# Kernel tuning notes

Measured on AMD Instinct MI355X. Metric: run time of the kernel, lower is better.

## Reference

```python
import jax, jax.numpy as jnp
import numpy as np

EPS = 1e-5

def _instance_norm(t):
    # torch .var(dim=2) default is unbiased (ddof=1) over flattened HW
    b, c, h, w = t.shape
    flat = t.reshape(b, c, h * w)
    mean = flat.mean(axis=2)
    var = flat.var(axis=2, ddof=1) + EPS
    return (t - mean[:, :, None, None]) / jnp.sqrt(var)[:, :, None, None]

def _conv1x1(t, w, b):
    # w: [Cout, Cin], b: [Cout]; t: [B, Cin, H, W]
    return jnp.einsum('oc,bchw->bohw', w, t) + b[None, :, None, None]


def setup_inputs() -> dict:
    key = jax.random.key(0)
    ks = jax.random.split(key, 11)
    B, C, H, W = 4, 512, 64, 64
    scale = 1.0 / np.sqrt(C)
    inp = {
        'c': jax.random.normal(ks[0], (B, C, H, W), jnp.float32),
        's': jax.random.normal(ks[1], (B, C, H, W), jnp.float32),
        'x': jax.random.normal(ks[2], (B, C, H, W), jnp.float32),
        'c_w': jax.random.normal(ks[3], (C, C), jnp.float32) * scale,
        'c_b': jax.random.normal(ks[4], (C,), jnp.float32) * 0.01,
        's_w': jax.random.normal(ks[5], (C, C), jnp.float32) * scale,
        's_b': jax.random.normal(ks[6], (C,), jnp.float32) * 0.01,
        'i_w': jax.random.normal(ks[7], (C, C), jnp.float32) * scale,
        'i_b': jax.random.normal(ks[8], (C,), jnp.float32) * 0.01,
        'o_w': jax.random.normal(ks[9], (C, C), jnp.float32) * scale,
        'o_b': jax.random.normal(ks[10], (C,), jnp.float32) * 0.01,
    }
    return inp


def reference(c, s, x, c_w, c_b, s_w, s_b, i_w, i_b, o_w, o_b):
    B, C, H, W = c.shape
    N = H * W
    cf = _conv1x1(_instance_norm(c), c_w, c_b).reshape(B, C, N)
    sf = _conv1x1(_instance_norm(s), s_w, s_b).reshape(B, C, N)
    xf = _conv1x1(s, i_w, i_b).reshape(B, C, N)
    # mask[b, n, m] = sum_c cf[b, c, n] * sf[b, c, m]; softmax over m
    mask = jax.nn.softmax(jnp.einsum('bcn,bcm->bnm', cf, sf), axis=-1)
    # of = xf @ mask^T : of[b, c, n] = sum_m xf[b, c, m] * mask[b, n, m]
    of = jnp.einsum('bcm,bnm->bcn', xf, mask).reshape(B, C, H, W)
    of = _conv1x1(of, o_w, o_b)
    return x + of
```

## Files before the change

kernel.cpp:

```cpp
#include <hip/hip_runtime.h>

typedef unsigned short u16;
typedef _Float16 f16x8 __attribute__((ext_vector_type(8)));
typedef float f32x4 __attribute__((ext_vector_type(4)));
typedef u16 u16x4 __attribute__((ext_vector_type(4)));
typedef u16 u16x8v __attribute__((ext_vector_type(8)));

__device__ __forceinline__ u16 f2h(float f) {
    _Float16 h = (_Float16)f;
    return __builtin_bit_cast(u16, h);
}
__device__ __forceinline__ float h2f(u16 u) {
    return (float)__builtin_bit_cast(_Float16, u);
}

__global__ void __launch_bounds__(256) stats_kernel(
    const float* __restrict__ c, const float* __restrict__ s,
    float* __restrict__ mC, float* __restrict__ rC,
    float* __restrict__ mS, float* __restrict__ rS)
{
    const float* src = (blockIdx.y ? s : c) + (size_t)blockIdx.x * 4096;
    int t = threadIdx.x, lane = t & 63, wv = t >> 6;
    const float4* p = (const float4*)src;
    float sum = 0.f, sq = 0.f;
#pragma unroll
    for (int i = 0; i < 4; ++i) {
        float4 v = p[t + 256 * i];
        sum += v.x + v.y + v.z + v.w;
        sq  += v.x * v.x + v.y * v.y + v.z * v.z + v.w * v.w;
    }
#pragma unroll
    for (int m = 1; m < 64; m <<= 1) {
        sum += __shfl_xor(sum, m);
        sq  += __shfl_xor(sq, m);
    }
    __shared__ float sa[4], sb[4];
    if (!lane) { sa[wv] = sum; sb[wv] = sq; }
    __syncthreads();
    if (t == 0) {
        float S = sa[0] + sa[1] + sa[2] + sa[3];
        float Q = sb[0] + sb[1] + sb[2] + sb[3];
        float mean = S * (1.0f / 4096.0f);
        float var = (Q - 4096.0f * mean * mean) * (1.0f / 4095.0f);
        float rstd = rsqrtf(var + 1e-5f);
        if (blockIdx.y) { mS[blockIdx.x] = mean; rS[blockIdx.x] = rstd; }
        else            { mC[blockIdx.x] = mean; rC[blockIdx.x] = rstd; }
    }
}

__global__ void __launch_bounds__(256) packall(
    const float* __restrict__ c, const float* __restrict__ s,
    const float* __restrict__ mC, const float* __restrict__ rC,
    const float* __restrict__ mS, const float* __restrict__ rS,
    u16* __restrict__ cnT, u16* __restrict__ snT, u16* __restrict__ sRT)
{
    __shared__ float tile[32][33];
    int z = blockIdx.z;
    bool isS = z >= 4;
    int b = isS ? z - 4 : z;
    const float* src  = isS ? s : c;
    const float* mean = isS ? mS : mC;
    const float* rstd = isS ? rS : rC;
    u16* dh = isS ? snT : cnT;
    int n0 = blockIdx.x * 32, c0 = blockIdx.y * 32;
    int tx = threadIdx.x, ty = threadIdx.y;
    const float* sbp = src + ((size_t)b * 512 + c0) * 4096 + n0;
#pragma unroll
    for (int it = 0; it < 4; ++it) {
        int cc = ty + it * 8;
        tile[cc][tx] = sbp[(size_t)cc * 4096 + tx];
    }
    __syncthreads();
    int ch = c0 + tx;
    float mn = mean[b * 512 + ch];
    float rs = rstd[b * 512 + ch];
    size_t obase = ((size_t)b * 4096 + n0) * 512 + c0;
#pragma unroll
    for (int it = 0; it < 4; ++it) {
        int r = ty + it * 8;
        float v = tile[tx][r];
        size_t o = obase + (size_t)r * 512 + tx;
        dh[o] = f2h((v - mn) * rs);
        if (isS) sRT[o] = f2h(v);
    }
}

__global__ void __launch_bounds__(256) prep_kernel(
    const float* __restrict__ c_w, const float* __restrict__ s_w,
    const float* __restrict__ i_w, const float* __restrict__ o_w,
    u16* __restrict__ cwT, u16* __restrict__ swT,
    u16* __restrict__ iwT, u16* __restrict__ ow)
{
    int z = blockIdx.z;
    int tx = threadIdx.x, ty = threadIdx.y;
    if (z == 3) {
        size_t base = ((size_t)(blockIdx.y * 16 + blockIdx.x) * 256 +
                       (ty * 32 + tx)) * 4;
        float4 v = *(const float4*)(o_w + base);
        u16x4 o;
        o[0] = f2h(v.x); o[1] = f2h(v.y); o[2] = f2h(v.z); o[3] = f2h(v.w);
        *(u16x4*)(ow + base) = o;
        return;
    }
    const float* w = (z == 0) ? c_w : (z == 1) ? s_w : i_w;
    u16* wT = (z == 0) ? cwT : (z == 1) ? swT : iwT;
    __shared__ float tile[32][33];
    int c0 = blockIdx.x * 32, k0 = blockIdx.y * 32;
#pragma unroll
    for (int it = 0; it < 4; ++it) {
        int kk = ty + it * 8;
        tile[kk][tx] = w[(size_t)(k0 + kk) * 512 + c0 + tx];
    }
    __syncthreads();
#pragma unroll
    for (int it = 0; it < 4; ++it) {
        int r = ty + it * 8;
        wT[(size_t)(c0 + r) * 512 + k0 + tx] = f2h(tile[tx][r]);
    }
}

__global__ void __launch_bounds__(256) bias_prep(
    const float* __restrict__ o_w, const float* __restrict__ i_b,
    const float* __restrict__ o_b, const float* __restrict__ s_w,
    const float* __restrict__ c_b, float* __restrict__ v,
    float* __restrict__ wu)
{
    __shared__ float buf[512];
    int t = threadIdx.x;
    bool isWu = blockIdx.x >= 2;
    const float* vec = isWu ? c_b : i_b;
    buf[t] = vec[t]; buf[t + 256] = vec[t + 256];
    __syncthreads();
    int o = (blockIdx.x & 1) * 256 + t;
    if (!isWu) {
        float acc = o_b[o];
        const float* row = o_w + (size_t)o * 512;
        for (int k = 0; k < 512; ++k) acc += row[k] * buf[k];
        v[o] = acc;
    } else {
        float acc = 0.f;
        for (int k = 0; k < 512; ++k) acc += buf[k] * s_w[(size_t)k * 512 + o];
        wu[o] = acc;
    }
}

__global__ void __launch_bounds__(256) rowdot_kernel(
    const u16* __restrict__ snT, const float* __restrict__ wu,
    float* __restrict__ u)
{
    __shared__ float swu[512];
    int t = threadIdx.x;
    swu[t] = wu[t]; swu[t + 256] = wu[t + 256];
    __syncthreads();
    int lane = t & 63, wv = t >> 6;
    int row = blockIdx.x * 4 + wv;
    u16x8v h = *(const u16x8v*)(snT + (size_t)row * 512 + lane * 8);
    float acc = 0.f;
#pragma unroll
    for (int i = 0; i < 8; ++i) acc += h2f(h[i]) * swu[lane * 8 + i];
#pragma unroll
    for (int m = 1; m < 64; m <<= 1) acc += __shfl_xor(acc, m);
    if (!lane) u[row] = acc;
}

#define EPI_F32       0
#define EPI_PLAIN_F16 2

__device__ __forceinline__ void stageA(
    const u16* __restrict__ g, int ldk, int i0, int k0, char* tile, int wv, int lane)
{
#pragma unroll
    for (int cc = 0; cc < 4; ++cc) {
        int chunk = (wv * 4 + cc) * 64 + lane;
        int row  = chunk >> 3;
        int slot = chunk & 7;
        int gc   = slot ^ (row & 7);
        const u16* gp = g + (size_t)(i0 + row) * ldk + (k0 + gc * 8);
        char* lp = tile + (size_t)(wv * 4 + cc) * 1024;
        __builtin_amdgcn_global_load_lds(
            (const __attribute__((address_space(1))) unsigned int*)gp,
            (__attribute__((address_space(3))) unsigned int*)lp, 16, 0, 0);
    }
}
__device__ __forceinline__ void stageB(
    const u16* __restrict__ g, int ldk, int j0, int k0, char* tile, int wv, int lane)
{
#pragma unroll
    for (int cc = 0; cc < 2; ++cc) {
        int chunk = (wv * 2 + cc) * 64 + lane;
        int row  = chunk >> 3;
        int slot = chunk & 7;
        int gc   = slot ^ (row & 7);
        const u16* gp = g + (size_t)(j0 + row) * ldk + (k0 + gc * 8);
        char* lp = tile + (size_t)(wv * 2 + cc) * 1024;
        __builtin_amdgcn_global_load_lds(
            (const __attribute__((address_space(1))) unsigned int*)gp,
            (__attribute__((address_space(3))) unsigned int*)lp, 16, 0, 0);
    }
}

template<int EPI>
__global__ void __launch_bounds__(512) gemm_bt(
    const u16* __restrict__ A_, const u16* __restrict__ B_,
    int K, int ldk, const float* __restrict__ bias,
    const float* __restrict__ jb, long jbZ,
    float* __restrict__ outF_, u16* __restrict__ outH_,
    int ldo, int zdiv,
    long aBatch, long aChunk, long bBatch, long bChunk, long oZ)
{
    __shared__ char smem[49152];

    int bz = blockIdx.z;
    int batch = bz / zdiv, chunk = bz % zdiv;
    const u16* A  = A_ + (size_t)batch * aBatch + (size_t)chunk * aChunk;
    const u16* Bm = B_ + (size_t)batch * bBatch + (size_t)chunk * bChunk;

    int i0 = blockIdx.y * 256, j0 = blockIdx.x * 128;
    int tid = threadIdx.x, lane = tid & 63, wv = tid >> 6;
    int wr = wv >> 1, wc = wv & 1;
    int r15 = lane & 15, h4 = lane >> 4;

    f32x4 zero = {0.f, 0.f, 0.f, 0.f};
    f32x4 acc[4][4];
#pragma unroll
    for (int m = 0; m < 4; ++m)
#pragma unroll
        for (int n = 0; n < 4; ++n) acc[m][n] = zero;

    for (int k0 = 0; k0 < K; k0 += 64) {
        stageA(A, ldk, i0, k0, smem, wv, lane);
        stageB(Bm, ldk, j0, k0, smem + 32768, wv, lane);
        asm volatile("s_waitcnt vmcnt(0)" ::: "memory");
        __syncthreads();
#pragma unroll
        for (int ks = 0; ks < 2; ++ks) {
            f16x8 a[4], b[4];
#pragma unroll
            for (int m = 0; m < 4; ++m) {
                int row = wr * 64 + m * 16 + r15;
                int off = row * 128 + (((ks * 4 + h4) ^ (row & 7)) << 4);
                a[m] = *(const f16x8*)(smem + off);
            }
#pragma unroll
            for (int n = 0; n < 4; ++n) {
                int col = wc * 64 + n * 16 + r15;
                int off = col * 128 + (((ks * 4 + h4) ^ (col & 7)) << 4);
                b[n] = *(const f16x8*)(smem + 32768 + off);
            }
#pragma unroll
            for (int m = 0; m < 4; ++m)
#pragma unroll
                for (int n = 0; n < 4; ++n)
                    acc[m][n] = __builtin_amdgcn_mfma_f32_16x16x32_f16(a[m], b[n], acc[m][n], 0, 0, 0);
        }
        __syncthreads();
    }

    float* outF = outF_ ? outF_ + (size_t)bz * oZ : nullptr;
    u16* outH = outH_ ? outH_ + (size_t)bz * oZ : nullptr;
    const float* jbp = jb ? jb + (size_t)bz * jbZ : nullptr;

#pragma unroll
    for (int m = 0; m < 4; ++m)
#pragma unroll
        for (int n = 0; n < 4; ++n) {
            int ibase = i0 + wr * 64 + m * 16 + h4 * 4;
            int j = j0 + wc * 64 + n * 16 + r15;
#pragma unroll
            for (int r = 0; r < 4; ++r) {
                int i = ibase + r;
                float v = acc[m][n][r];
                if constexpr (EPI == EPI_PLAIN_F16) {
                    if (bias) v += bias[i];
                    if (jbp) v += jbp[j];
                    outH[(size_t)i * ldo + j] = f2h(v);
                } else {
                    outF[(size_t)i * ldo + j] = v;
                }
            }
        }
}

__global__ void __launch_bounds__(256) softmax16(u16* __restrict__ LP)
{
    u16x8v* row = (u16x8v*)(LP + (size_t)blockIdx.x * 4096);
    int t = threadIdx.x, lane = t & 63, wv = t >> 6;
    u16x8v ca = row[t], cb = row[t + 256];
    float va[8], vb[8];
    float mx = -3.4e38f;
#pragma unroll
    for (int i = 0; i < 8; ++i) {
        va[i] = h2f(ca[i]); vb[i] = h2f(cb[i]);
        mx = fmaxf(mx, fmaxf(va[i], vb[i]));
    }
#pragma unroll
    for (int m = 1; m < 64; m <<= 1) mx = fmaxf(mx, __shfl_xor(mx, m));
    __shared__ float sM[4], sS[4];
    if (!lane) sM[wv] = mx;
    __syncthreads();
    mx = fmaxf(fmaxf(sM[0], sM[1]), fmaxf(sM[2], sM[3]));
    float sum = 0.f;
#pragma unroll
    for (int i = 0; i < 8; ++i) {
        va[i] = __expf(va[i] - mx);
        vb[i] = __expf(vb[i] - mx);
        sum += va[i] + vb[i];
    }
#pragma unroll
    for (int m = 1; m < 64; m <<= 1) sum += __shfl_xor(sum, m);
    if (!lane) sS[wv] = sum;
    __syncthreads();
    sum = sS[0] + sS[1] + sS[2] + sS[3];
    float inv = 1.0f / sum;
    u16x8v oa, ob;
#pragma unroll
    for (int i = 0; i < 8; ++i) {
        oa[i] = f2h(va[i] * inv);
        ob[i] = f2h(vb[i] * inv);
    }
    row[t] = oa; row[t + 256] = ob;
}

__global__ void __launch_bounds__(256) reduce4resid(
    const u16* __restrict__ part, const float* __restrict__ xr,
    const float* __restrict__ v, float* __restrict__ out)
{
    const size_t PLANE = 2097152;
    int b = blockIdx.y;
    size_t g8 = ((size_t)blockIdx.x * 256 + threadIdx.x) * 8;
    const u16* p0 = part + (size_t)b * 4 * PLANE + g8;
    float acc[8] = {0.f, 0.f, 0.f, 0.f, 0.f, 0.f, 0.f, 0.f};
#pragma unroll
    for (int k = 0; k < 4; ++k) {
        u16x8v h = *(const u16x8v*)(p0 + (size_t)k * PLANE);
#pragma unroll
        for (int i = 0; i < 8; ++i) acc[i] += h2f(h[i]);
    }
    const float4* xv = (const float4*)(xr + (size_t)b * PLANE + g8);
    float4 x0 = xv[0], x1 = xv[1];
    float vc = v[g8 >> 12];
    float4 o0, o1;
    o0.x = acc[0] + x0.x + vc; o0.y = acc[1] + x0.y + vc;
    o0.z = acc[2] + x0.z + vc; o0.w = acc[3] + x0.w + vc;
    o1.x = acc[4] + x1.x + vc; o1.y = acc[5] + x1.y + vc;
    o1.z = acc[6] + x1.z + vc; o1.w = acc[7] + x1.w + vc;
    float4* op = (float4*)(out + (size_t)b * PLANE + g8);
    op[0] = o0; op[1] = o1;
}

extern "C" void kernel_launch(void* const* d_in, const int* in_sizes, int n_in,
                              void* d_out, int out_size, void* d_ws, size_t ws_size,
                              hipStream_t stream)
{
    const float* c   = (const float*)d_in[0];
    const float* s   = (const float*)d_in[1];
    const float* x   = (const float*)d_in[2];
    const float* c_w = (const float*)d_in[3];
    const float* c_b = (const float*)d_in[4];
    const float* s_w = (const float*)d_in[5];
    const float* s_b = (const float*)d_in[6];
    const float* i_w = (const float*)d_in[7];
    const float* i_b = (const float*)d_in[8];
    const float* o_w = (const float*)d_in[9];
    const float* o_b = (const float*)d_in[10];
    float* out = (float*)d_out;
    char* ws = (char*)d_ws;

    const int B = 4, C = 512, N = 4096;
    const size_t NC = (size_t)N * C;
    const size_t W2 = (size_t)C * C;
    const size_t NN = (size_t)N * N;

    size_t off = 0;
    auto alloc = [&](size_t bytes) { size_t o = off; off += (bytes + 255) & ~(size_t)255; return o; };

    size_t o_meanC = alloc((size_t)B * C * 4);
    size_t o_rstdC = alloc((size_t)B * C * 4);
    size_t o_meanS = alloc((size_t)B * C * 4);
    size_t o_rstdS = alloc((size_t)B * C * 4);
    size_t o_cwT = alloc(W2 * 2);
    size_t o_swT = alloc(W2 * 2);
    size_t o_iwT = alloc(W2 * 2);
    size_t o_ow  = alloc(W2 * 2);
    size_t o_G   = alloc(W2 * 2);
    size_t o_W   = alloc(W2 * 2);
    size_t o_v   = alloc((size_t)C * 4);
    size_t o_wu  = alloc((size_t)C * 4);
    size_t o_u   = alloc((size_t)B * N * 4);
    size_t o_cnT = alloc(B * NC * 2);
    size_t o_snT = alloc(B * NC * 2);
    size_t o_sRT = alloc(B * NC * 2);
    size_t o_sgT = alloc(B * NC * 2);
    size_t o_sW  = alloc(B * NC * 2);
    size_t o_P   = alloc(2 * NN * 2);
    size_t o_pt  = alloc(8 * NC * 2);

    if (ws_size < off) {
        (void)hipMemsetAsync(d_out, 0, (size_t)out_size * 4, stream);
        return;
    }

    float* meanC = (float*)(ws + o_meanC);
    float* rstdC = (float*)(ws + o_rstdC);
    float* meanS = (float*)(ws + o_meanS);
    float* rstdS = (float*)(ws + o_rstdS);
    u16* cwT = (u16*)(ws + o_cwT);
    u16* swT = (u16*)(ws + o_swT);
    u16* iwT = (u16*)(ws + o_iwT);
    u16* ow  = (u16*)(ws + o_ow);
    u16* Gf  = (u16*)(ws + o_G);
    u16* Wf  = (u16*)(ws + o_W);
    float* vb = (float*)(ws + o_v);
    float* wu = (float*)(ws + o_wu);
    float* ub = (float*)(ws + o_u);
    u16* cnT = (u16*)(ws + o_cnT);
    u16* snT = (u16*)(ws + o_snT);
    u16* sRT = (u16*)(ws + o_sRT);
    u16* sgT = (u16*)(ws + o_sgT);
    u16* sW  = (u16*)(ws + o_sW);
    u16* Pb  = (u16*)(ws + o_P);
    u16* partH = (u16*)(ws + o_pt);

    stats_kernel<<<dim3(B * C, 2), 256, 0, stream>>>(c, s, meanC, rstdC, meanS, rstdS);
    packall<<<dim3(N / 32, C / 32, 8), dim3(32, 8), 0, stream>>>(
        c, s, meanC, rstdC, meanS, rstdS, cnT, snT, sRT);
    prep_kernel<<<dim3(16, 16, 4), dim3(32, 8), 0, stream>>>(
        c_w, s_w, i_w, o_w, cwT, swT, iwT, ow);
    bias_prep<<<dim3(4), 256, 0, stream>>>(o_w, i_b, o_b, s_w, c_b, vb, wu);
    gemm_bt<EPI_PLAIN_F16><<<dim3(4, 2, 2), 512, 0, stream>>>(
        cwT, swT, 512, 512, nullptr, nullptr, 0, nullptr, Gf, 512, 1,
        (long)(3 * W2), 0, (long)W2, 0, (long)W2);
    gemm_bt<EPI_PLAIN_F16><<<dim3(4, 16, B), 512, 0, stream>>>(
        snT, Gf, 512, 512, nullptr, nullptr, 0, nullptr, sgT, 512, 1,
        (long)NC, 0, 0, 0, (long)NC);
    gemm_bt<EPI_PLAIN_F16><<<dim3(32, 2, B), 512, 0, stream>>>(
        Wf, sRT, 512, 512, nullptr, nullptr, 0, nullptr, sW, 4096, 1,
        0, 0, (long)NC, 0, (long)NC);
    rowdot_kernel<<<dim3(B * N / 4), 256, 0, stream>>>(snT, wu, ub);
    for (int pb0 = 0; pb0 < B; pb0 += 2) {
        gemm_bt<EPI_PLAIN_F16><<<dim3(32, 16, 2), 512, 0, stream>>>(
            cnT + (size_t)pb0 * NC, sgT + (size_t)pb0 * NC,
            512, 512, nullptr, ub + (size_t)pb0 * N, (long)N,
            nullptr, Pb, 4096, 1,
            (long)NC, 0, (long)NC, 0, (long)NN);
        softmax16<<<dim3(2 * N), 256, 0, stream>>>(Pb);
        gemm_bt<EPI_PLAIN_F16><<<dim3(32, 2, 8), 512, 0, stream>>>(
            sW + (size_t)pb0 * NC, Pb, 1024, 4096, nullptr, nullptr, 0,
            nullptr, partH, 4096, 4,
            (long)NC, 1024L, (long)NN, 1024L, (long)NC);
        reduce4resid<<<dim3((int)(NC / 2048), 2), 256, 0, stream>>>(
            partH, x + (size_t)pb0 * NC, vb, out + (size_t)pb0 * NC);
    }
}
```

Baseline: 350.6 us.

## Triple-buffer GEMM shared-memory tiles with async global-to-LDS prefetch

Replaces the single-buffered K loop in gemm_bt with a three-slot ring of LDS tiles, prefetching two K-steps ahead via global_load_lds and waiting with partial vmcnt counts. The goal is to overlap global memory latency with the MFMA compute, which the old loop serialized by waiting on vmcnt(0) each iteration. LDS use grows to 144KB of dynamic shared memory per block, which limits occupancy to one 512-thread block per CU and depends on the vmcnt counts matching the number of loads issued per stage.

```diff
diff --git a/kernel.cpp b/kernel.cpp
--- a/kernel.cpp
+++ b/kernel.cpp
@@ -165,6 +165,7 @@
 
 #define EPI_F32       0
 #define EPI_PLAIN_F16 2
+#define SLOT 49152
 
 __device__ __forceinline__ void stageA(
     const u16* __restrict__ g, int ldk, int i0, int k0, char* tile, int wv, int lane)
@@ -208,7 +209,7 @@
     int ldo, int zdiv,
     long aBatch, long aChunk, long bBatch, long bChunk, long oZ)
 {
-    __shared__ char smem[49152];
+    extern __shared__ char smem[];
 
     int bz = blockIdx.z;
     int batch = bz / zdiv, chunk = bz % zdiv;
@@ -227,10 +228,29 @@
 #pragma unroll
         for (int n = 0; n < 4; ++n) acc[m][n] = zero;
 
-    for (int k0 = 0; k0 < K; k0 += 64) {
-        stageA(A, ldk, i0, k0, smem, wv, lane);
-        stageB(Bm, ldk, j0, k0, smem + 32768, wv, lane);
-        asm volatile("s_waitcnt vmcnt(0)" ::: "memory");
+    int nk = K >> 6;
+    stageA(A, ldk, i0, 0, smem, wv, lane);
+    stageB(Bm, ldk, j0, 0, smem + 32768, wv, lane);
+    if (nk > 1) {
+        stageA(A, ldk, i0, 64, smem + SLOT, wv, lane);
+        stageB(Bm, ldk, j0, 64, smem + SLOT + 32768, wv, lane);
+    }
+
+    int cs = 0, ns = 2;
+    for (int t = 0; t < nk; ++t) {
+        char* sAc = smem + cs * SLOT;
+        char* sBc = sAc + 32768;
+        if (t + 2 < nk) {
+            char* sS = smem + ns * SLOT;
+            stageA(A, ldk, i0, (t + 2) * 64, sS, wv, lane);
+            stageB(Bm, ldk, j0, (t + 2) * 64, sS + 32768, wv, lane);
+            asm volatile("s_waitcnt vmcnt(12)" ::: "memory");
+            ns = (ns == 2) ? 0 : ns + 1;
+        } else if (t + 1 < nk) {
+            asm volatile("s_waitcnt vmcnt(6)" ::: "memory");
+        } else {
+            asm volatile("s_waitcnt vmcnt(0)" ::: "memory");
+        }
         __syncthreads();
 #pragma unroll
         for (int ks = 0; ks < 2; ++ks) {
@@ -239,13 +259,13 @@
             for (int m = 0; m < 4; ++m) {
                 int row = wr * 64 + m * 16 + r15;
                 int off = row * 128 + (((ks * 4 + h4) ^ (row & 7)) << 4);
-                a[m] = *(const f16x8*)(smem + off);
+                a[m] = *(const f16x8*)(sAc + off);
             }
 #pragma unroll
             for (int n = 0; n < 4; ++n) {
                 int col = wc * 64 + n * 16 + r15;
                 int off = col * 128 + (((ks * 4 + h4) ^ (col & 7)) << 4);
-                b[n] = *(const f16x8*)(smem + 32768 + off);
+                b[n] = *(const f16x8*)(sBc + off);
             }
 #pragma unroll
             for (int m = 0; m < 4; ++m)
@@ -254,6 +274,7 @@
                     acc[m][n] = __builtin_amdgcn_mfma_f32_16x16x32_f16(a[m], b[n], acc[m][n], 0, 0, 0);
         }
         __syncthreads();
+        cs = (cs == 2) ? 0 : cs + 1;
     }
 
     float* outF = outF_ ? outF_ + (size_t)bz * oZ : nullptr;
@@ -370,6 +391,7 @@
     const size_t NC = (size_t)N * C;
     const size_t W2 = (size_t)C * C;
     const size_t NN = (size_t)N * N;
+    const int SMEM = 3 * SLOT;
 
     size_t off = 0;
     auto alloc = [&](size_t bytes) { size_t o = off; off += (bytes + 255) & ~(size_t)255; return o; };
@@ -427,24 +449,24 @@
     prep_kernel<<<dim3(16, 16, 4), dim3(32, 8), 0, stream>>>(
         c_w, s_w, i_w, o_w, cwT, swT, iwT, ow);
     bias_prep<<<dim3(4), 256, 0, stream>>>(o_w, i_b, o_b, s_w, c_b, vb, wu);
-    gemm_bt<EPI_PLAIN_F16><<<dim3(4, 2, 2), 512, 0, stream>>>(
+    gemm_bt<EPI_PLAIN_F16><<<dim3(4, 2, 2), 512, SMEM, stream>>>(
         cwT, swT, 512, 512, nullptr, nullptr, 0, nullptr, Gf, 512, 1,
         (long)(3 * W2), 0, (long)W2, 0, (long)W2);
-    gemm_bt<EPI_PLAIN_F16><<<dim3(4, 16, B), 512, 0, stream>>>(
+    gemm_bt<EPI_PLAIN_F16><<<dim3(4, 16, B), 512, SMEM, stream>>>(
         snT, Gf, 512, 512, nullptr, nullptr, 0, nullptr, sgT, 512, 1,
         (long)NC, 0, 0, 0, (long)NC);
-    gemm_bt<EPI_PLAIN_F16><<<dim3(32, 2, B), 512, 0, stream>>>(
+    gemm_bt<EPI_PLAIN_F16><<<dim3(32, 2, B), 512, SMEM, stream>>>(
         Wf, sRT, 512, 512, nullptr, nullptr, 0, nullptr, sW, 4096, 1,
         0, 0, (long)NC, 0, (long)NC);
     rowdot_kernel<<<dim3(B * N / 4), 256, 0, stream>>>(snT, wu, ub);
     for (int pb0 = 0; pb0 < B; pb0 += 2) {
-        gemm_bt<EPI_PLAIN_F16><<<dim3(32, 16, 2), 512, 0, stream>>>(
+        gemm_bt<EPI_PLAIN_F16><<<dim3(32, 16, 2), 512, SMEM, stream>>>(
             cnT + (size_t)pb0 * NC, sgT + (size_t)pb0 * NC,
             512, 512, nullptr, ub + (size_t)pb0 * N, (long)N,
             nullptr, Pb, 4096, 1,
             (long)NC, 0, (long)NC, 0, (long)NN);
         softmax16<<<dim3(2 * N), 256, 0, stream>>>(Pb);
-        gemm_bt<EPI_PLAIN_F16><<<dim3(32, 2, 8), 512, 0, stream>>>(
+        gemm_bt<EPI_PLAIN_F16><<<dim3(32, 2, 8), 512, SMEM, stream>>>(
             sW + (size_t)pb0 * NC, Pb, 1024, 4096, nullptr, nullptr, 0,
             nullptr, partH, 4096, 4,
             (long)NC, 1024L, (long)NN, 1024L, (long)NC);
```

Measured after the change: 438.0 us. 1.25x slower.

## Add 256x256 double-buffered GEMM with direct global-to-LDS loads for attention GEMMs

Applied to the files above, without the earlier changes.

Introduces a new gemm8p kernel with 256x256 output tiles per block. It double-buffers 64-wide K slices in 128KB of dynamic LDS, filled by global_load_lds with an XOR swizzle. Next-slice loads are interleaved per quadrant with vmcnt waits and setprio to overlap memory with MFMA work. The two large attention GEMMs (score and output) switch to it, which raises per-block arithmetic intensity and cuts LDS staging overhead. In exchange it uses more LDS and registers, leaves fewer blocks in the grid, and makes dynamic shared memory above 64KB a requirement.

```diff
diff --git a/kernel.cpp b/kernel.cpp
--- a/kernel.cpp
+++ b/kernel.cpp
@@ -279,6 +279,137 @@
                 }
             }
         }
+}
+
+__device__ __forceinline__ void stageHalf8(
+    const u16* __restrict__ g, int ldk, int row0, int k0, char* dst,
+    int wv, int lane)
+{
+#pragma unroll
+    for (int cc = 0; cc < 2; ++cc) {
+        int chunk = wv * 64 + lane + cc * 512;
+        int row  = chunk >> 3;
+        int slot = chunk & 7;
+        int gc   = slot ^ (row & 7);
+        const u16* gp = g + (size_t)(row0 + row) * ldk + (k0 + gc * 8);
+        char* lp = dst + (size_t)(wv * 64 + cc * 512) * 16;
+        __builtin_amdgcn_global_load_lds(
+            (const __attribute__((address_space(1))) unsigned int*)gp,
+            (__attribute__((address_space(3))) unsigned int*)lp, 16, 0, 0);
+    }
+}
+
+__global__ void __launch_bounds__(512) gemm8p(
+    const u16* __restrict__ A_, const u16* __restrict__ B_,
+    int K, int ldk, const float* __restrict__ bias,
+    const float* __restrict__ jb, long jbZ,
+    u16* __restrict__ outH_, int ldo, int zdiv,
+    long aBatch, long aChunk, long bBatch, long bChunk, long oZ)
+{
+    extern __shared__ char smem[];
+
+    int bz = blockIdx.z;
+    int batch = bz / zdiv, chunk = bz % zdiv;
+    const u16* A  = A_ + (size_t)batch * aBatch + (size_t)chunk * aChunk;
+    const u16* Bm = B_ + (size_t)batch * bBatch + (size_t)chunk * bChunk;
+
+    int i0 = blockIdx.y * 256, j0 = blockIdx.x * 256;
+    int tid = threadIdx.x, lane = tid & 63, wv = tid >> 6;
+    int wr = wv >> 2, wc2 = wv & 3;
+    int r15 = lane & 15, h4 = lane >> 4;
+
+    f32x4 zero = {0.f, 0.f, 0.f, 0.f};
+    f32x4 acc[4][4][2];
+#pragma unroll
+    for (int q = 0; q < 4; ++q)
+#pragma unroll
+        for (int m = 0; m < 4; ++m)
+#pragma unroll
+            for (int n = 0; n < 2; ++n) acc[q][m][n] = zero;
+
+    int nk = K >> 6;
+    stageHalf8(A,  ldk, i0,       0, smem,                 wv, lane);
+    stageHalf8(Bm, ldk, j0,       0, smem + 32768,         wv, lane);
+    stageHalf8(Bm, ldk, j0 + 128, 0, smem + 32768 + 16384, wv, lane);
+    stageHalf8(A,  ldk, i0 + 128, 0, smem + 16384,         wv, lane);
+    asm volatile("s_waitcnt vmcnt(0)" ::: "memory");
+    __builtin_amdgcn_s_barrier();
+    asm volatile("" ::: "memory");
+
+    for (int t = 0; t < nk; ++t) {
+        char* bufA = smem + (t & 1) * 65536;
+        char* bufB = bufA + 32768;
+        char* nbuf = smem + ((t + 1) & 1) * 65536;
+#pragma unroll
+        for (int q = 0; q < 4; ++q) {
+            const int mi = (q >= 2) ? 1 : 0;
+            const int ni = (q == 1 || q == 2) ? 1 : 0;
+            if (t + 1 < nk) {
+                int k0 = (t + 1) * 64;
+                if (q == 0)      stageHalf8(A,  ldk, i0,       k0, nbuf,                 wv, lane);
+                else if (q == 1) stageHalf8(Bm, ldk, j0,       k0, nbuf + 32768,         wv, lane);
+                else if (q == 2) stageHalf8(Bm, ldk, j0 + 128, k0, nbuf + 32768 + 16384, wv, lane);
+                else             stageHalf8(A,  ldk, i0 + 128, k0, nbuf + 16384,         wv, lane);
+                if (q < 3) asm volatile("s_waitcnt vmcnt(6)" ::: "memory");
+            } else {
+                if (q == 0)      asm volatile("s_waitcnt vmcnt(4)" ::: "memory");
+                else if (q == 1) asm volatile("s_waitcnt vmcnt(2)" ::: "memory");
+                else if (q == 2) asm volatile("s_waitcnt vmcnt(0)" ::: "memory");
+            }
+            __builtin_amdgcn_s_barrier();
+            asm volatile("" ::: "memory");
+            __builtin_amdgcn_sched_barrier(0);
+            __builtin_amdgcn_s_setprio(1);
+#pragma unroll
+            for (int ks = 0; ks < 2; ++ks) {
+                f16x8 a[4], b[2];
+#pragma unroll
+                for (int m = 0; m < 4; ++m) {
+                    int row = mi * 128 + wr * 64 + m * 16 + r15;
+                    int off = row * 128 + (((ks * 4 + h4) ^ (row & 7)) << 4);
+                    a[m] = *(const f16x8*)(bufA + off);
+                }
+#pragma unroll
+                for (int n = 0; n < 2; ++n) {
+                    int col = ni * 128 + wc2 * 32 + n * 16 + r15;
+                    int off = col * 128 + (((ks * 4 + h4) ^ (col & 7)) << 4);
+                    b[n] = *(const f16x8*)(bufB + off);
+                }
+#pragma unroll
+                for (int m = 0; m < 4; ++m)
+#pragma unroll
+                    for (int n = 0; n < 2; ++n)
+                        acc[q][m][n] = __builtin_amdgcn_mfma_f32_16x16x32_f16(a[m], b[n], acc[q][m][n], 0, 0, 0);
+            }
+            __builtin_amdgcn_s_setprio(0);
+            __builtin_amdgcn_sched_barrier(0);
+            asm volatile("" ::: "memory");
+            __builtin_amdgcn_s_barrier();
+        }
+    }
+
+    u16* outH = outH_ + (size_t)bz * oZ;
+    const float* jbp = jb ? jb + (size_t)bz * jbZ : nullptr;
+#pragma unroll
+    for (int q = 0; q < 4; ++q) {
+        const int mi = (q >= 2) ? 1 : 0;
+        const int ni = (q == 1 || q == 2) ? 1 : 0;
+#pragma unroll
+        for (int m = 0; m < 4; ++m)
+#pragma unroll
+            for (int n = 0; n < 2; ++n) {
+                int ibase = i0 + mi * 128 + wr * 64 + m * 16 + h4 * 4;
+                int j = j0 + ni * 128 + wc2 * 32 + n * 16 + r15;
+#pragma unroll
+                for (int r = 0; r < 4; ++r) {
+                    int i = ibase + r;
+                    float v = acc[q][m][n][r];
+                    if (bias) v += bias[i];
+                    if (jbp) v += jbp[j];
+                    outH[(size_t)i * ldo + j] = f2h(v);
+                }
+            }
+    }
 }
 
 __global__ void __launch_bounds__(256) softmax16(u16* __restrict__ LP)
@@ -370,6 +501,7 @@
     const size_t NC = (size_t)N * C;
     const size_t W2 = (size_t)C * C;
     const size_t NN = (size_t)N * N;
+    const int SMEM8 = 131072;
 
     size_t off = 0;
     auto alloc = [&](size_t bytes) { size_t o = off; off += (bytes + 255) & ~(size_t)255; return o; };
@@ -438,15 +570,15 @@
         0, 0, (long)NC, 0, (long)NC);
     rowdot_kernel<<<dim3(B * N / 4), 256, 0, stream>>>(snT, wu, ub);
     for (int pb0 = 0; pb0 < B; pb0 += 2) {
-        gemm_bt<EPI_PLAIN_F16><<<dim3(32, 16, 2), 512, 0, stream>>>(
+        gemm8p<<<dim3(16, 16, 2), 512, SMEM8, stream>>>(
             cnT + (size_t)pb0 * NC, sgT + (size_t)pb0 * NC,
             512, 512, nullptr, ub + (size_t)pb0 * N, (long)N,
-            nullptr, Pb, 4096, 1,
+            Pb, 4096, 1,
             (long)NC, 0, (long)NC, 0, (long)NN);
         softmax16<<<dim3(2 * N), 256, 0, stream>>>(Pb);
-        gemm_bt<EPI_PLAIN_F16><<<dim3(32, 2, 8), 512, 0, stream>>>(
+        gemm8p<<<dim3(16, 2, 8), 512, SMEM8, stream>>>(
             sW + (size_t)pb0 * NC, Pb, 1024, 4096, nullptr, nullptr, 0,
-            nullptr, partH, 4096, 4,
+            partH, 4096, 4,
             (long)NC, 1024L, (long)NN, 1024L, (long)NC);
         reduce4resid<<<dim3((int)(NC / 2048), 2), 256, 0, stream>>>(
             partH, x + (size_t)pb0 * NC, vb, out + (size_t)pb0 * NC);
```

Result: slower. 395.7 us (+12.9%).

## Add dedicated 256x256-tile logits GEMM with direct global-to-LDS loads

Applied to the files above, without the earlier changes.

Replaces the generic gemm_bt call for the attention logits with a specialized kernel that computes 256x256 output tiles per block, using global_load_lds async copies into a 64KB XOR-swizzled shared tile and 8x4 MFMA accumulators per wave. Larger tiles raise operand reuse and halve the number of blocks loading A and B. The trade-off is higher register pressure, 64KB of LDS per block (lower occupancy), and no double buffering, since each k-step waits on vmcnt(0) before computing.

```diff
diff --git a/kernel.cpp b/kernel.cpp
--- a/kernel.cpp
+++ b/kernel.cpp
@@ -277,6 +277,93 @@
                 } else {
                     outF[(size_t)i * ldo + j] = v;
                 }
+            }
+        }
+}
+
+__device__ __forceinline__ void stage256(
+    const u16* __restrict__ g, int r0, int k0, char* tile, int wv, int lane)
+{
+#pragma unroll
+    for (int cc = 0; cc < 4; ++cc) {
+        int grp = cc * 8 + wv;
+        int chunk = grp * 64 + lane;
+        int row  = chunk >> 3;
+        int slot = chunk & 7;
+        int gc   = slot ^ (row & 7);
+        const u16* gp = g + (size_t)(r0 + row) * 512 + (k0 + gc * 8);
+        char* lp = tile + (size_t)grp * 1024;
+        __builtin_amdgcn_global_load_lds(
+            (const __attribute__((address_space(1))) unsigned int*)gp,
+            (__attribute__((address_space(3))) unsigned int*)lp, 16, 0, 0);
+    }
+}
+
+__global__ void __launch_bounds__(512) glogits256(
+    const u16* __restrict__ A_, const u16* __restrict__ B_,
+    const float* __restrict__ jb_, u16* __restrict__ outH_,
+    long aZ, long bZ, long jbZ, long oZ)
+{
+    extern __shared__ char smem[];
+
+    int bz = blockIdx.z;
+    const u16* A  = A_ + (size_t)bz * aZ;
+    const u16* Bm = B_ + (size_t)bz * bZ;
+
+    int i0 = blockIdx.y * 256, j0 = blockIdx.x * 256;
+    int tid = threadIdx.x, lane = tid & 63, wv = tid >> 6;
+    int wr = wv >> 2, wc = wv & 3;
+    int r15 = lane & 15, h4 = lane >> 4;
+
+    f32x4 zero = {0.f, 0.f, 0.f, 0.f};
+    f32x4 acc[8][4];
+#pragma unroll
+    for (int m = 0; m < 8; ++m)
+#pragma unroll
+        for (int n = 0; n < 4; ++n) acc[m][n] = zero;
+
+    for (int k0 = 0; k0 < 512; k0 += 64) {
+        stage256(A,  i0, k0, smem,         wv, lane);
+        stage256(Bm, j0, k0, smem + 32768, wv, lane);
+        asm volatile("s_waitcnt vmcnt(0)" ::: "memory");
+        __syncthreads();
+#pragma unroll
+        for (int ks = 0; ks < 2; ++ks) {
+            f16x8 a[8], b[4];
+#pragma unroll
+            for (int m = 0; m < 8; ++m) {
+                int row = wr * 128 + m * 16 + r15;
+                int off = row * 128 + (((ks * 4 + h4) ^ (row & 7)) << 4);
+                a[m] = *(const f16x8*)(smem + off);
+            }
+#pragma unroll
+            for (int n = 0; n < 4; ++n) {
+                int col = wc * 64 + n * 16 + r15;
+                int off = col * 128 + (((ks * 4 + h4) ^ (col & 7)) << 4);
+                b[n] = *(const f16x8*)(smem + 32768 + off);
+            }
+#pragma unroll
+            for (int m = 0; m < 8; ++m)
+#pragma unroll
+                for (int n = 0; n < 4; ++n)
+                    acc[m][n] = __builtin_amdgcn_mfma_f32_16x16x32_f16(a[m], b[n], acc[m][n], 0, 0, 0);
+        }
+        __syncthreads();
+    }
+
+    u16* outH = outH_ + (size_t)bz * oZ;
+    const float* jbp = jb_ + (size_t)bz * jbZ;
+#pragma unroll
+    for (int m = 0; m < 8; ++m)
+#pragma unroll
+        for (int n = 0; n < 4; ++n) {
+            int ibase = i0 + wr * 128 + m * 16 + h4 * 4;
+            int j = j0 + wc * 64 + n * 16 + r15;
+            float ub = jbp[j];
+#pragma unroll
+            for (int r = 0; r < 4; ++r) {
+                int i = ibase + r;
+                outH[(size_t)i * 4096 + j] = f2h(acc[m][n][r] + ub);
             }
         }
 }
@@ -370,6 +457,7 @@
     const size_t NC = (size_t)N * C;
     const size_t W2 = (size_t)C * C;
     const size_t NN = (size_t)N * N;
+    const int SMEM256 = 65536;
 
     size_t off = 0;
     auto alloc = [&](size_t bytes) { size_t o = off; off += (bytes + 255) & ~(size_t)255; return o; };
@@ -438,11 +526,10 @@
         0, 0, (long)NC, 0, (long)NC);
     rowdot_kernel<<<dim3(B * N / 4), 256, 0, stream>>>(snT, wu, ub);
     for (int pb0 = 0; pb0 < B; pb0 += 2) {
-        gemm_bt<EPI_PLAIN_F16><<<dim3(32, 16, 2), 512, 0, stream>>>(
+        glogits256<<<dim3(16, 16, 2), 512, SMEM256, stream>>>(
             cnT + (size_t)pb0 * NC, sgT + (size_t)pb0 * NC,
-            512, 512, nullptr, ub + (size_t)pb0 * N, (long)N,
-            nullptr, Pb, 4096, 1,
-            (long)NC, 0, (long)NC, 0, (long)NN);
+            ub + (size_t)pb0 * N, Pb,
+            (long)NC, (long)NC, (long)N, (long)NN);
         softmax16<<<dim3(2 * N), 256, 0, stream>>>(Pb);
         gemm_bt<EPI_PLAIN_F16><<<dim3(32, 2, 8), 512, 0, stream>>>(
             sW + (size_t)pb0 * NC, Pb, 1024, 4096, nullptr, nullptr, 0,
```

Measured after the change: 339.8 us. 3.1% less time.
